# Kernel tuning notes

Measured on AMD Instinct MI355X. Metric: run time of the kernel, lower is better.

## Reference

```python
import jax, jax.numpy as jnp
import numpy as np

N_NODES = 100000
N_EDGES = 3200000
N_FEAT = 128
N_GRAPHS = 512
BN_EPS = 1e-5


def setup_inputs() -> dict:
    key = jax.random.key(0)
    ks = jax.random.split(key, 16)
    x = jax.random.normal(ks[0], (N_NODES, N_FEAT), dtype=jnp.float32)
    edge_index = jax.random.randint(ks[1], (2, N_EDGES), 0, N_NODES, dtype=jnp.int32)
    batch = jnp.sort(jax.random.randint(ks[2], (N_NODES,), 0, N_GRAPHS, dtype=jnp.int32))
    def lin(k, fi, fo):
        s = 1.0 / np.sqrt(fi)
        return jax.random.uniform(k, (fi, fo), jnp.float32, -s, s)
    return {
        "x": x,
        "edge_index": edge_index,
        "batch": batch,
        # conv1: GraphConv(128 -> 30): lin_rel (with bias) + lin_root (no bias)
        "W_rel1": lin(ks[3], N_FEAT, 30),
        "W_root1": lin(ks[4], N_FEAT, 30),
        "b1": jnp.zeros((30,), jnp.float32),
        "bn1_g": jnp.ones((30,), jnp.float32),
        "bn1_b": jnp.zeros((30,), jnp.float32),
        "bn1_m": jnp.zeros((30,), jnp.float32),
        "bn1_v": jnp.ones((30,), jnp.float32),
        # conv2: GraphConv(30 -> 20)
        "W_rel2": lin(ks[5], 30, 20),
        "W_root2": lin(ks[6], 30, 20),
        "b2": jnp.zeros((20,), jnp.float32),
        "bn2_g": jnp.ones((20,), jnp.float32),
        "bn2_b": jnp.zeros((20,), jnp.float32),
        "bn2_m": jnp.zeros((20,), jnp.float32),
        "bn2_v": jnp.ones((20,), jnp.float32),
        # head
        "W_lin1": lin(ks[7], 40, 10),
        "b_lin1": jnp.zeros((10,), jnp.float32),
        "W_lin2": lin(ks[8], 10, 1),
        "b_lin2": jnp.zeros((1,), jnp.float32),
    }


def _bn(h, g, b, m, v):
    return (h - m) * jax.lax.rsqrt(v + BN_EPS) * g + b


def reference(x, edge_index, batch,
              W_rel1, W_root1, b1, bn1_g, bn1_b, bn1_m, bn1_v,
              W_rel2, W_root2, b2, bn2_g, bn2_b, bn2_m, bn2_v,
              W_lin1, b_lin1, W_lin2, b_lin2):
    n = x.shape[0]
    src, dst = edge_index[0], edge_index[1]
    # ---- GraphConv 1: out = aggr_add(x_src -> dst) @ W_rel + x @ W_root + b
    agg = jax.ops.segment_sum(x[src], dst, num_segments=n)  # [N,128]
    h = jax.nn.relu(agg @ W_rel1 + x @ W_root1 + b1)        # [N,30]
    h = _bn(h, bn1_g, bn1_b, bn1_m, bn1_v)
    # ---- GraphConv 2
    agg2 = jax.ops.segment_sum(h[src], dst, num_segments=n)  # [N,30]
    h2 = jax.nn.relu(agg2 @ W_rel2 + h @ W_root2 + b2)       # [N,20]
    h2 = _bn(h2, bn2_g, bn2_b, bn2_m, bn2_v)
    # ---- global pools over graph ids
    gmax = jax.ops.segment_max(h2, batch, num_segments=N_GRAPHS)  # [G,20]
    gmax = jnp.where(jnp.isfinite(gmax), gmax, 0.0)
    gsum = jax.ops.segment_sum(h2, batch, num_segments=N_GRAPHS)
    cnt = jax.ops.segment_sum(jnp.ones((n,), h2.dtype), batch, num_segments=N_GRAPHS)
    gmean = gsum / jnp.maximum(cnt, 1.0)[:, None]
    z = jnp.concatenate([gmax, gmean], axis=1)               # [G,40]
    z = jax.nn.relu(z @ W_lin1 + b_lin1)
    return jax.nn.sigmoid(z @ W_lin2 + b_lin2)               # [G,1]
```

## Files before the change

kernel.cpp:

```cpp
#include <hip/hip_runtime.h>
#include <math.h>

#define NFEAT 128
#define F1    30
#define F1P   32
#define F2    20

#define EPB     8192
#define MAXBUCK 1024

__global__ __launch_bounds__(256) void k_prepw(
    const float* __restrict__ Wrel, const float* __restrict__ Wroot,
    float* __restrict__ Wp)
{
    int i = blockIdx.x * 256 + threadIdx.x;
    if (i >= 2 * 128 * 32) return;
    int table = i >> 12, rem = i & 4095, k = rem >> 5, j = rem & 31;
    const float* W = table ? Wroot : Wrel;
    Wp[i] = (j < F1) ? W[k * F1 + j] : 0.f;
}

__global__ __launch_bounds__(512) void k_proj1(
    const float* __restrict__ x, const float* __restrict__ Wp,
    float* __restrict__ y1, float* __restrict__ r1, int n)
{
    __shared__ float4 xs4[2048];
    int tid = threadIdx.x;
    int base = blockIdx.x * 64;

#pragma unroll
    for (int it = 0; it < 4; it++) {
        int idx = it * 512 + tid;
        int k4 = idx & 31, row = idx >> 5;
        int gnode = base + row;
        float4 v = make_float4(0.f, 0.f, 0.f, 0.f);
        if (gnode < n) v = ((const float4*)(x + (size_t)gnode * NFEAT))[k4];
        xs4[k4 * 64 + (row ^ k4)] = v;
    }
    __syncthreads();

    int lane = tid & 63;
    int combo = __builtin_amdgcn_readfirstlane(tid >> 6);
    int table = combo >> 2, q = combo & 3;
    int node = base + lane;
    if (node >= n) return;

    const float* Wt = Wp + table * 4096 + q * 8;
    float acc[8];
#pragma unroll
    for (int j = 0; j < 8; j++) acc[j] = 0.f;

    for (int k4 = 0; k4 < 32; k4++) {
        float4 xk = xs4[k4 * 64 + (lane ^ k4)];
#pragma unroll
        for (int kk = 0; kk < 4; kk++) {
            float xs = kk == 0 ? xk.x : kk == 1 ? xk.y : kk == 2 ? xk.z : xk.w;
            const float* w = Wt + (k4 * 4 + kk) * 32;
            acc[0] += xs * w[0]; acc[1] += xs * w[1];
            acc[2] += xs * w[2]; acc[3] += xs * w[3];
            acc[4] += xs * w[4]; acc[5] += xs * w[5];
            acc[6] += xs * w[6]; acc[7] += xs * w[7];
        }
    }
    float* outp = (table ? r1 : y1) + (size_t)node * F1P + q * 8;
    ((float4*)outp)[0] = make_float4(acc[0], acc[1], acc[2], acc[3]);
    ((float4*)outp)[1] = make_float4(acc[4], acc[5], acc[6], acc[7]);
}

__global__ __launch_bounds__(256) void k_p1(
    const int* __restrict__ ei, int* __restrict__ blockCnt,
    int E, int nbuck)
{
    __shared__ int lh[MAXBUCK];
    int t = threadIdx.x;
    for (int i = t; i < nbuck; i += 256) lh[i] = 0;
    __syncthreads();
    const int* dst = ei + E;
    int base = blockIdx.x * EPB;
#pragma unroll 4
    for (int k = 0; k < EPB / 256; k++) {
        int e = base + k * 256 + t;
        if (e < E) atomicAdd(&lh[dst[e] >> 7], 1);
    }
    __syncthreads();
    int* out = blockCnt + (size_t)blockIdx.x * nbuck;
    for (int i = t; i < nbuck; i += 256) out[i] = lh[i];
}

__global__ __launch_bounds__(256) void k_p2(
    const int* __restrict__ blockCnt, int* __restrict__ blockOff,
    int* __restrict__ bucketTot, int neb, int nbuck)
{
    __shared__ int sdata[256];
    __shared__ int carry_s;
    int b = blockIdx.x;
    int t = threadIdx.x;
    if (t == 0) carry_s = 0;
    __syncthreads();
    for (int base = 0; base < neb; base += 512) {
        int i0 = base + 2 * t, i1 = i0 + 1;
        int c0 = (i0 < neb) ? blockCnt[(size_t)i0 * nbuck + b] : 0;
        int c1 = (i1 < neb) ? blockCnt[(size_t)i1 * nbuck + b] : 0;
        int s = c0 + c1;
        sdata[t] = s;
        __syncthreads();
        for (int off = 1; off < 256; off <<= 1) {
            int tmp = (t >= off) ? sdata[t - off] : 0;
            __syncthreads();
            sdata[t] += tmp;
            __syncthreads();
        }
        int ex = carry_s + sdata[t] - s;
        if (i0 < neb) blockOff[(size_t)i0 * nbuck + b] = ex;
        if (i1 < neb) blockOff[(size_t)i1 * nbuck + b] = ex + c0;
        __syncthreads();
        if (t == 255) carry_s += sdata[255];
        __syncthreads();
    }
    if (t == 0) bucketTot[b] = carry_s;
}

__global__ __launch_bounds__(256) void k_p3(
    const int* __restrict__ bucketTot, int* __restrict__ bucketStart, int nbuck)
{
    __shared__ int sdata[256];
    __shared__ int carry_s;
    int t = threadIdx.x;
    if (t == 0) carry_s = 0;
    __syncthreads();
    for (int base = 0; base < nbuck; base += 1024) {
        int v[4]; int s = 0;
#pragma unroll
        for (int i = 0; i < 4; i++) {
            int idx = base + t * 4 + i;
            v[i] = (idx < nbuck) ? bucketTot[idx] : 0;
            s += v[i];
        }
        sdata[t] = s;
        __syncthreads();
        for (int off = 1; off < 256; off <<= 1) {
            int tmp = (t >= off) ? sdata[t - off] : 0;
            __syncthreads();
            sdata[t] += tmp;
            __syncthreads();
        }
        int ex = carry_s + sdata[t] - s;
#pragma unroll
        for (int i = 0; i < 4; i++) {
            int idx = base + t * 4 + i;
            if (idx < nbuck) bucketStart[idx] = ex;
            ex += v[i];
        }
        __syncthreads();
        if (t == 255) carry_s += sdata[255];
        __syncthreads();
    }
    if (t == 0) bucketStart[nbuck] = carry_s;
}

__global__ __launch_bounds__(256) void k_p4(
    const int* __restrict__ ei, const int* __restrict__ bucketStart,
    const int* __restrict__ blockOff, int* __restrict__ ebuf,
    int E, int nbuck)
{
    __shared__ int cur[MAXBUCK];
    int t = threadIdx.x;
    const int* boff = blockOff + (size_t)blockIdx.x * nbuck;
    for (int i = t; i < nbuck; i += 256) cur[i] = bucketStart[i] + boff[i];
    __syncthreads();
    const int* dst = ei + E;
    int base = blockIdx.x * EPB;
#pragma unroll 4
    for (int k = 0; k < EPB / 256; k++) {
        int e = base + k * 256 + t;
        if (e < E) {
            int s = ei[e], d = dst[e];
            int p = atomicAdd(&cur[d >> 7], 1);
            ebuf[p] = (s << 7) | (d & 127);
        }
    }
}

__global__ __launch_bounds__(256) void k_p5(
    const int* __restrict__ ebuf, const int* __restrict__ bucketStart,
    int* __restrict__ deg, int n)
{
    __shared__ int nh[128];
    int t = threadIdx.x;
    int b = blockIdx.x;
    if (t < 128) nh[t] = 0;
    __syncthreads();
    int lo = bucketStart[b], hi = bucketStart[b + 1];
    for (int p = lo + t; p < hi; p += 256)
        atomicAdd(&nh[ebuf[p] & 127], 1);
    __syncthreads();
    if (t < 128) {
        int node = b * 128 + t;
        if (node < n) deg[node] = nh[t];
    }
}

__global__ __launch_bounds__(256) void k_scan1(
    const int* __restrict__ deg, int* __restrict__ bsum, int n)
{
    __shared__ int sdata[256];
    int t = threadIdx.x;
    int base = blockIdx.x * 1024;
    int s = 0;
#pragma unroll
    for (int i = 0; i < 4; i++) {
        int idx = base + t * 4 + i;
        if (idx < n) s += deg[idx];
    }
    sdata[t] = s;
    __syncthreads();
    for (int off = 128; off > 0; off >>= 1) {
        if (t < off) sdata[t] += sdata[t + off];
        __syncthreads();
    }
    if (t == 0) bsum[blockIdx.x] = sdata[0];
}

__global__ void k_scan2(const int* __restrict__ bsum, int* __restrict__ boff, int nb)
{
    if (threadIdx.x == 0 && blockIdx.x == 0) {
        int acc = 0;
        for (int i = 0; i < nb; i++) { boff[i] = acc; acc += bsum[i]; }
    }
}

__global__ __launch_bounds__(256) void k_scan3(
    const int* __restrict__ deg, const int* __restrict__ boff,
    int* __restrict__ rowstart, int n)
{
    __shared__ int sdata[256];
    int t = threadIdx.x;
    int base = blockIdx.x * 1024;
    int v[4]; int s = 0;
#pragma unroll
    for (int i = 0; i < 4; i++) {
        int idx = base + t * 4 + i;
        v[i] = (idx < n) ? deg[idx] : 0;
        s += v[i];
    }
    sdata[t] = s;
    __syncthreads();
    for (int off = 1; off < 256; off <<= 1) {
        int tmp = (t >= off) ? sdata[t - off] : 0;
        __syncthreads();
        sdata[t] += tmp;
        __syncthreads();
    }
    int ex = boff[blockIdx.x] + sdata[t] - s;
#pragma unroll
    for (int i = 0; i < 4; i++) {
        int idx = base + t * 4 + i;
        if (idx < n) rowstart[idx] = ex;
        ex += v[i];
    }
}

__global__ __launch_bounds__(256) void k_p6(
    const int* __restrict__ ebuf, const int* __restrict__ bucketStart,
    const int* __restrict__ rowstart, int* __restrict__ perm, int n,
    int t1, int t2, int t3)
{
    __shared__ int cur[128];
    int t = threadIdx.x;
    int b = blockIdx.x;
    if (t < 128) {
        int node = b * 128 + t;
        cur[t] = (node < n) ? rowstart[node] : 0;
    }
    __syncthreads();
    int lo = bucketStart[b], hi = bucketStart[b + 1];
    for (int pass = 0; pass < 4; pass++) {
        for (int p = lo + t; p < hi; p += 256) {
            int e = ebuf[p];
            int src = e >> 7;
            int qq = (src >= t1) + (src >= t2) + (src >= t3);
            if (qq == pass) {
                int q = atomicAdd(&cur[e & 127], 1);
                perm[q] = src;
            }
        }
        __syncthreads();
    }
}

__global__ __launch_bounds__(256) void k_agg1(
    const int* __restrict__ rowstart, const int* __restrict__ deg,
    const int* __restrict__ perm, const float* __restrict__ y1,
    float* __restrict__ agg1, int n)
{
    int idx = blockIdx.x * 256 + threadIdx.x;
    int node = idx >> 3, q = idx & 7;
    if (node >= n) return;
    int s = rowstart[node], e = s + deg[node];
    float4 acc = {0.f, 0.f, 0.f, 0.f};
    int j = s;
    for (; j + 4 <= e; j += 4) {
        int s0 = perm[j], s1 = perm[j + 1], s2 = perm[j + 2], s3 = perm[j + 3];
        float4 v0 = *(const float4*)(y1 + (size_t)s0 * F1P + q * 4);
        float4 v1 = *(const float4*)(y1 + (size_t)s1 * F1P + q * 4);
        float4 v2 = *(const float4*)(y1 + (size_t)s2 * F1P + q * 4);
        float4 v3 = *(const float4*)(y1 + (size_t)s3 * F1P + q * 4);
        acc.x += v0.x; acc.y += v0.y; acc.z += v0.z; acc.w += v0.w;
        acc.x += v1.x; acc.y += v1.y; acc.z += v1.z; acc.w += v1.w;
        acc.x += v2.x; acc.y += v2.y; acc.z += v2.z; acc.w += v2.w;
        acc.x += v3.x; acc.y += v3.y; acc.z += v3.z; acc.w += v3.w;
    }
    for (; j < e; j++) {
        int sr = perm[j];
        float4 v = *(const float4*)(y1 + (size_t)sr * F1P + q * 4);
        acc.x += v.x; acc.y += v.y; acc.z += v.z; acc.w += v.w;
    }
    *(float4*)(agg1 + (size_t)node * F1P + q * 4) = acc;
}

__global__ __launch_bounds__(256) void k_agg2(
    const int* __restrict__ rowstart, const int* __restrict__ deg,
    const int* __restrict__ perm, const float* __restrict__ y2,
    float* __restrict__ agg2, int n)
{
    int idx = blockIdx.x * 256 + threadIdx.x;
    int node = idx / 5, q = idx - node * 5;
    if (node >= n) return;
    int s = rowstart[node], e = s + deg[node];
    float4 acc = {0.f, 0.f, 0.f, 0.f};
    int j = s;
    for (; j + 4 <= e; j += 4) {
        int s0 = perm[j], s1 = perm[j + 1], s2 = perm[j + 2], s3 = perm[j + 3];
        float4 v0 = *(const float4*)(y2 + (size_t)s0 * F2 + q * 4);
        float4 v1 = *(const float4*)(y2 + (size_t)s1 * F2 + q * 4);
        float4 v2 = *(const float4*)(y2 + (size_t)s2 * F2 + q * 4);
        float4 v3 = *(const float4*)(y2 + (size_t)s3 * F2 + q * 4);
        acc.x += v0.x; acc.y += v0.y; acc.z += v0.z; acc.w += v0.w;
        acc.x += v1.x; acc.y += v1.y; acc.z += v1.z; acc.w += v1.w;
        acc.x += v2.x; acc.y += v2.y; acc.z += v2.z; acc.w += v2.w;
        acc.x += v3.x; acc.y += v3.y; acc.z += v3.z; acc.w += v3.w;
    }
    for (; j < e; j++) {
        int sr = perm[j];
        float4 v = *(const float4*)(y2 + (size_t)sr * F2 + q * 4);
        acc.x += v.x; acc.y += v.y; acc.z += v.z; acc.w += v.w;
    }
    *(float4*)(agg2 + (size_t)node * F2 + q * 4) = acc;
}

__global__ __launch_bounds__(256) void k_mid(
    const float* __restrict__ agg1, const float* __restrict__ r1,
    const float* __restrict__ b1,
    const float* __restrict__ g1, const float* __restrict__ bb1,
    const float* __restrict__ m1, const float* __restrict__ v1,
    const float* __restrict__ Wrel2, const float* __restrict__ Wroot2,
    const float* __restrict__ b2,
    float* __restrict__ y2, float* __restrict__ r2, int n)
{
    int node = blockIdx.x * 256 + threadIdx.x;
    if (node >= n) return;
    float h[F1];
    const float4* av = (const float4*)(agg1 + (size_t)node * F1P);
    const float4* rv = (const float4*)(r1   + (size_t)node * F1P);
#pragma unroll
    for (int q = 0; q < 8; q++) {
        float4 a = av[q], r = rv[q];
        int j = q * 4;
        if (j + 0 < F1) h[j + 0] = a.x + r.x;
        if (j + 1 < F1) h[j + 1] = a.y + r.y;
        if (j + 2 < F1) h[j + 2] = a.z + r.z;
        if (j + 3 < F1) h[j + 3] = a.w + r.w;
    }
#pragma unroll
    for (int j = 0; j < F1; j++) {
        float t = fmaxf(h[j] + b1[j], 0.f);
        float sc = g1[j] / sqrtf(v1[j] + 1e-5f);
        h[j] = (t - m1[j]) * sc + bb1[j];
    }
    float ay[F2], ar[F2];
#pragma unroll
    for (int j = 0; j < F2; j++) { ay[j] = 0.f; ar[j] = b2[j]; }
    for (int k = 0; k < F1; k++) {
        float hk = h[k];
#pragma unroll
        for (int j = 0; j < F2; j++) {
            ay[j] += hk * Wrel2 [k * F2 + j];
            ar[j] += hk * Wroot2[k * F2 + j];
        }
    }
    float4* yo = (float4*)(y2 + (size_t)node * F2);
    float4* ro = (float4*)(r2 + (size_t)node * F2);
#pragma unroll
    for (int q = 0; q < 5; q++) {
        float4 vy, vr;
        vy.x = ay[q*4+0]; vy.y = ay[q*4+1]; vy.z = ay[q*4+2]; vy.w = ay[q*4+3];
        vr.x = ar[q*4+0]; vr.y = ar[q*4+1]; vr.z = ar[q*4+2]; vr.w = ar[q*4+3];
        yo[q] = vy;  ro[q] = vr;
    }
}

__global__ __launch_bounds__(256) void k_pool(
    const float* __restrict__ agg2, const float* __restrict__ r2,
    const int* __restrict__ batch,
    const float* __restrict__ g2, const float* __restrict__ bb2,
    const float* __restrict__ m2, const float* __restrict__ v2,
    unsigned* __restrict__ gmaxU, float* __restrict__ gsum,
    int* __restrict__ cnt, int n)
{
    int t = threadIdx.x;
    if (t >= 240) return;
    int i = t / 20, j = t - (t / 20) * 20;
    int base = blockIdx.x * 256;
    int nend = min(base + 256, n);
    float sc = g2[j] / sqrtf(v2[j] + 1e-5f);
    float mj = m2[j], bj = bb2[j];

    int curg = -1, c = 0;
    float mx = -3.4e38f, sm = 0.f;
    for (int node = base + i; node < nend; node += 12) {
        int g = batch[node];
        if (g != curg) {
            if (curg >= 0) {
                atomicAdd(&gsum[curg * F2 + j], sm);
                unsigned bits = __float_as_uint(mx);
                unsigned mapped = (bits & 0x80000000u) ? ~bits : (bits | 0x80000000u);
                atomicMax(&gmaxU[curg * F2 + j], mapped);
                if (j == 0) atomicAdd(&cnt[curg], c);
            }
            curg = g; c = 0; mx = -3.4e38f; sm = 0.f;
        }
        float a = agg2[(size_t)node * F2 + j] + r2[(size_t)node * F2 + j];
        a = fmaxf(a, 0.f);
        float h2 = (a - mj) * sc + bj;
        mx = fmaxf(mx, h2); sm += h2; c++;
    }
    if (curg >= 0) {
        atomicAdd(&gsum[curg * F2 + j], sm);
        unsigned bits = __float_as_uint(mx);
        unsigned mapped = (bits & 0x80000000u) ? ~bits : (bits | 0x80000000u);
        atomicMax(&gmaxU[curg * F2 + j], mapped);
        if (j == 0) atomicAdd(&cnt[curg], c);
    }
}

__global__ __launch_bounds__(256) void k_head(
    const unsigned* __restrict__ gmaxU, const float* __restrict__ gsum,
    const int* __restrict__ cnt,
    const float* __restrict__ W1, const float* __restrict__ b1h,
    const float* __restrict__ W2, const float* __restrict__ b2h,
    float* __restrict__ out, int G)
{
    int g = blockIdx.x * 256 + threadIdx.x;
    if (g >= G) return;
    int c = cnt[g];
    float cf = fmaxf((float)c, 1.f);
    float z[2 * F2];
#pragma unroll
    for (int j = 0; j < F2; j++) {
        unsigned u = gmaxU[g * F2 + j];
        float gm = 0.f;
        if (c != 0) {
            gm = (u & 0x80000000u) ? __uint_as_float(u & 0x7FFFFFFFu)
                                   : __uint_as_float(~u);
            if (!isfinite(gm)) gm = 0.f;
        }
        z[j]      = gm;
        z[F2 + j] = gsum[g * F2 + j] / cf;
    }
    float a[10];
#pragma unroll
    for (int i = 0; i < 10; i++) a[i] = b1h[i];
    for (int k = 0; k < 2 * F2; k++) {
        float zk = z[k];
#pragma unroll
        for (int i = 0; i < 10; i++) a[i] += zk * W1[k * 10 + i];
    }
    float o = b2h[0];
#pragma unroll
    for (int i = 0; i < 10; i++) o += fmaxf(a[i], 0.f) * W2[i];
    out[g] = 1.f / (1.f + expf(-o));
}

extern "C" void kernel_launch(void* const* d_in, const int* in_sizes, int n_in,
                              void* d_out, int out_size, void* d_ws, size_t ws_size,
                              hipStream_t stream)
{
    const float* x      = (const float*)d_in[0];
    const int*   ei     = (const int*)  d_in[1];
    const int*   batch  = (const int*)  d_in[2];
    const float* Wrel1  = (const float*)d_in[3];
    const float* Wroot1 = (const float*)d_in[4];
    const float* b1     = (const float*)d_in[5];
    const float* bn1_g  = (const float*)d_in[6];
    const float* bn1_b  = (const float*)d_in[7];
    const float* bn1_m  = (const float*)d_in[8];
    const float* bn1_v  = (const float*)d_in[9];
    const float* Wrel2  = (const float*)d_in[10];
    const float* Wroot2 = (const float*)d_in[11];
    const float* b2     = (const float*)d_in[12];
    const float* bn2_g  = (const float*)d_in[13];
    const float* bn2_b  = (const float*)d_in[14];
    const float* bn2_m  = (const float*)d_in[15];
    const float* bn2_v  = (const float*)d_in[16];
    const float* W_lin1 = (const float*)d_in[17];
    const float* b_lin1 = (const float*)d_in[18];
    const float* W_lin2 = (const float*)d_in[19];
    const float* b_lin2 = (const float*)d_in[20];
    float* out = (float*)d_out;

    int n = in_sizes[0] / NFEAT;
    int E = in_sizes[1] / 2;
    int G = out_size;
    int nb = (n + 1023) / 1024;
    int nbuck = (n + 127) >> 7;
    int neb = (E + EPB - 1) / EPB;
    int qs = (n + 3) >> 2;

    char* p = (char*)d_ws;
    float* y1   = (float*)p;  p += (size_t)n * F1P * 4;
    float* r1   = (float*)p;  p += (size_t)n * F1P * 4;
    char* alias0 = p;
    float* agg1 = (float*)p;  p += (size_t)n * F1P * 4;
    float* y2   = (float*)p;  p += (size_t)n * F2 * 4;
    float* r2   = (float*)p;  p += (size_t)n * F2 * 4;
    char* alias1 = p;
    float* agg2 = (float*)p;  p += (size_t)n * F2 * 4;
    unsigned* gmaxU = (unsigned*)p;  p += (size_t)G * F2 * 4;
    float*    gsum  = (float*)p;     p += (size_t)G * F2 * 4;
    int*      cnt   = (int*)p;       p += (size_t)G * 4;
    int* deg      = (int*)p;  p += (size_t)n * 4;
    int* rowstart = (int*)p;  p += (size_t)n * 4;
    int* bsum     = (int*)p;  p += (size_t)nb * 4;
    int* boff     = (int*)p;  p += (size_t)nb * 4;
    int* perm     = (int*)p;  p += (size_t)E * 4;
    float* Wp     = (float*)p; p += 2 * 128 * 32 * 4;

    int* ebuf = (int*)alias0;
    int* blockCnt    = (int*)alias1;
    int* blockOff    = blockCnt + (size_t)neb * nbuck;
    int* bucketTot   = blockOff + (size_t)neb * nbuck;
    int* bucketStart = bucketTot + nbuck;

    hipMemsetAsync(gmaxU, 0, (size_t)G * (F2 * 4 * 2 + 4), stream);

    k_p1<<<neb, 256, 0, stream>>>(ei, blockCnt, E, nbuck);
    k_p2<<<nbuck, 256, 0, stream>>>(blockCnt, blockOff, bucketTot, neb, nbuck);
    k_p3<<<1, 256, 0, stream>>>(bucketTot, bucketStart, nbuck);
    k_p4<<<neb, 256, 0, stream>>>(ei, bucketStart, blockOff, ebuf, E, nbuck);
    k_p5<<<nbuck, 256, 0, stream>>>(ebuf, bucketStart, deg, n);
    k_scan1<<<nb, 256, 0, stream>>>(deg, bsum, n);
    k_scan2<<<1, 64, 0, stream>>>(bsum, boff, nb);
    k_scan3<<<nb, 256, 0, stream>>>(deg, boff, rowstart, n);
    k_p6<<<nbuck, 256, 0, stream>>>(ebuf, bucketStart, rowstart, perm, n,
                                    qs, 2 * qs, 3 * qs);

    k_prepw<<<32, 256, 0, stream>>>(Wrel1, Wroot1, Wp);
    k_proj1<<<(n + 63) / 64, 512, 0, stream>>>(x, Wp, y1, r1, n);
    k_agg1<<<(n * 8 + 255) / 256, 256, 0, stream>>>(rowstart, deg, perm, y1, agg1, n);
    k_mid<<<(n + 255) / 256, 256, 0, stream>>>(agg1, r1, b1, bn1_g, bn1_b, bn1_m,
                                               bn1_v, Wrel2, Wroot2, b2, y2, r2, n);
    k_agg2<<<(n * 5 + 255) / 256, 256, 0, stream>>>(rowstart, deg, perm, y2, agg2, n);
    k_pool<<<(n + 255) / 256, 256, 0, stream>>>(agg2, r2, batch, bn2_g, bn2_b,
                                                bn2_m, bn2_v, gmaxU, gsum, cnt, n);
    k_head<<<(G + 255) / 256, 256, 0, stream>>>(gmaxU, gsum, cnt, W_lin1, b_lin1,
                                                W_lin2, b_lin2, out, G);
}
```

Measured before the change: 421.6 us.

## Replace global bucket sort with per-block local sort and transposed offsets

```diff
diff --git a/kernel.cpp b/kernel.cpp
--- a/kernel.cpp
+++ b/kernel.cpp
@@ -67,132 +67,87 @@
     ((float4*)outp)[1] = make_float4(acc[4], acc[5], acc[6], acc[7]);
 }
 
-__global__ __launch_bounds__(256) void k_p1(
-    const int* __restrict__ ei, int* __restrict__ blockCnt,
-    int E, int nbuck)
+__global__ __launch_bounds__(512) void k_sort(
+    const int* __restrict__ ei, int* __restrict__ ebuf,
+    int* __restrict__ rowScan, int E, int nbuck)
 {
     __shared__ int lh[MAXBUCK];
+    __shared__ int sdata[512];
     int t = threadIdx.x;
-    for (int i = t; i < nbuck; i += 256) lh[i] = 0;
-    __syncthreads();
+    int base = blockIdx.x * EPB;
+    const int* src = ei;
     const int* dst = ei + E;
-    int base = blockIdx.x * EPB;
+
+    for (int i = t; i < MAXBUCK; i += 512) lh[i] = 0;
+    __syncthreads();
 #pragma unroll 4
-    for (int k = 0; k < EPB / 256; k++) {
-        int e = base + k * 256 + t;
+    for (int k = 0; k < EPB / 512; k++) {
+        int e = base + k * 512 + t;
         if (e < E) atomicAdd(&lh[dst[e] >> 7], 1);
     }
     __syncthreads();
-    int* out = blockCnt + (size_t)blockIdx.x * nbuck;
-    for (int i = t; i < nbuck; i += 256) out[i] = lh[i];
-}
-
-__global__ __launch_bounds__(256) void k_p2(
-    const int* __restrict__ blockCnt, int* __restrict__ blockOff,
-    int* __restrict__ bucketTot, int neb, int nbuck)
-{
-    __shared__ int sdata[256];
-    __shared__ int carry_s;
-    int b = blockIdx.x;
-    int t = threadIdx.x;
-    if (t == 0) carry_s = 0;
-    __syncthreads();
-    for (int base = 0; base < neb; base += 512) {
-        int i0 = base + 2 * t, i1 = i0 + 1;
-        int c0 = (i0 < neb) ? blockCnt[(size_t)i0 * nbuck + b] : 0;
-        int c1 = (i1 < neb) ? blockCnt[(size_t)i1 * nbuck + b] : 0;
-        int s = c0 + c1;
-        sdata[t] = s;
+    int v0 = lh[2 * t], v1 = lh[2 * t + 1];
+    int pairSum = v0 + v1;
+    sdata[t] = pairSum;
+    __syncthreads();
+    for (int off = 1; off < 512; off <<= 1) {
+        int tmp = (t >= off) ? sdata[t - off] : 0;
         __syncthreads();
-        for (int off = 1; off < 256; off <<= 1) {
-            int tmp = (t >= off) ? sdata[t - off] : 0;
-            __syncthreads();
-            sdata[t] += tmp;
-            __syncthreads();
-        }
-        int ex = carry_s + sdata[t] - s;
-        if (i0 < neb) blockOff[(size_t)i0 * nbuck + b] = ex;
-        if (i1 < neb) blockOff[(size_t)i1 * nbuck + b] = ex + c0;
+        sdata[t] += tmp;
         __syncthreads();
-        if (t == 255) carry_s += sdata[255];
-        __syncthreads();
-    }
-    if (t == 0) bucketTot[b] = carry_s;
-}
-
-__global__ __launch_bounds__(256) void k_p3(
-    const int* __restrict__ bucketTot, int* __restrict__ bucketStart, int nbuck)
-{
-    __shared__ int sdata[256];
-    __shared__ int carry_s;
-    int t = threadIdx.x;
-    if (t == 0) carry_s = 0;
-    __syncthreads();
-    for (int base = 0; base < nbuck; base += 1024) {
-        int v[4]; int s = 0;
-#pragma unroll
-        for (int i = 0; i < 4; i++) {
-            int idx = base + t * 4 + i;
-            v[i] = (idx < nbuck) ? bucketTot[idx] : 0;
-            s += v[i];
-        }
-        sdata[t] = s;
-        __syncthreads();
-        for (int off = 1; off < 256; off <<= 1) {
-            int tmp = (t >= off) ? sdata[t - off] : 0;
-            __syncthreads();
-            sdata[t] += tmp;
-            __syncthreads();
-        }
-        int ex = carry_s + sdata[t] - s;
-#pragma unroll
-        for (int i = 0; i < 4; i++) {
-            int idx = base + t * 4 + i;
-            if (idx < nbuck) bucketStart[idx] = ex;
-            ex += v[i];
-        }
-        __syncthreads();
-        if (t == 255) carry_s += sdata[255];
-        __syncthreads();
-    }
-    if (t == 0) bucketStart[nbuck] = carry_s;
-}
-
-__global__ __launch_bounds__(256) void k_p4(
-    const int* __restrict__ ei, const int* __restrict__ bucketStart,
-    const int* __restrict__ blockOff, int* __restrict__ ebuf,
-    int E, int nbuck)
-{
-    __shared__ int cur[MAXBUCK];
-    int t = threadIdx.x;
-    const int* boff = blockOff + (size_t)blockIdx.x * nbuck;
-    for (int i = t; i < nbuck; i += 256) cur[i] = bucketStart[i] + boff[i];
-    __syncthreads();
-    const int* dst = ei + E;
-    int base = blockIdx.x * EPB;
+    }
+    int exPair = sdata[t] - pairSum;
+    lh[2 * t] = exPair;
+    lh[2 * t + 1] = exPair + v0;
+    __syncthreads();
+    int* rs = rowScan + (size_t)blockIdx.x * (nbuck + 1);
+    for (int i = t; i < nbuck + 1; i += 512) rs[i] = lh[i];
+    __syncthreads();
+    int* out = ebuf + (size_t)base;
 #pragma unroll 4
-    for (int k = 0; k < EPB / 256; k++) {
-        int e = base + k * 256 + t;
+    for (int k = 0; k < EPB / 512; k++) {
+        int e = base + k * 512 + t;
         if (e < E) {
-            int s = ei[e], d = dst[e];
-            int p = atomicAdd(&cur[d >> 7], 1);
-            ebuf[p] = (s << 7) | (d & 127);
-        }
+            int s = src[e], d = dst[e];
+            int p = atomicAdd(&lh[d >> 7], 1);
+            out[p] = (s << 7) | (d & 127);
+        }
+    }
+}
+
+__global__ __launch_bounds__(256) void k_t(
+    const int* __restrict__ in, int* __restrict__ out, int rows, int cols)
+{
+    __shared__ int tile[32][33];
+    int cb = blockIdx.x * 32, rb = blockIdx.y * 32;
+    for (int i = threadIdx.y; i < 32; i += 8) {
+        int r = rb + i, c = cb + threadIdx.x;
+        if (r < rows && c < cols) tile[i][threadIdx.x] = in[(size_t)r * cols + c];
+    }
+    __syncthreads();
+    for (int i = threadIdx.y; i < 32; i += 8) {
+        int c = cb + i, r = rb + threadIdx.x;
+        if (c < cols && r < rows) out[(size_t)c * rows + r] = tile[threadIdx.x][i];
     }
 }
 
 __global__ __launch_bounds__(256) void k_p5(
-    const int* __restrict__ ebuf, const int* __restrict__ bucketStart,
-    int* __restrict__ deg, int n)
+    const int* __restrict__ ebuf, const int* __restrict__ rsT,
+    int* __restrict__ deg, int n, int neb)
 {
     __shared__ int nh[128];
     int t = threadIdx.x;
     int b = blockIdx.x;
     if (t < 128) nh[t] = 0;
     __syncthreads();
-    int lo = bucketStart[b], hi = bucketStart[b + 1];
-    for (int p = lo + t; p < hi; p += 256)
-        atomicAdd(&nh[ebuf[p] & 127], 1);
+    const int* r0 = rsT + (size_t)b * neb;
+    const int* r1 = rsT + (size_t)(b + 1) * neb;
+    for (int blk = t; blk < neb; blk += 256) {
+        int lo = blk * EPB + r0[blk];
+        int hi = blk * EPB + r1[blk];
+        for (int p = lo; p < hi; p++)
+            atomicAdd(&nh[ebuf[p] & 127], 1);
+    }
     __syncthreads();
     if (t < 128) {
         int node = b * 128 + t;
@@ -261,9 +216,9 @@
 }
 
 __global__ __launch_bounds__(256) void k_p6(
-    const int* __restrict__ ebuf, const int* __restrict__ bucketStart,
-    const int* __restrict__ rowstart, int* __restrict__ perm, int n,
-    int t1, int t2, int t3)
+    const int* __restrict__ ebuf, const int* __restrict__ rsT,
+    const int* __restrict__ rowstart, int* __restrict__ perm,
+    int n, int neb, float inv8)
 {
     __shared__ int cur[128];
     int t = threadIdx.x;
@@ -272,14 +227,28 @@
         int node = b * 128 + t;
         cur[t] = (node < n) ? rowstart[node] : 0;
     }
-    __syncthreads();
-    int lo = bucketStart[b], hi = bucketStart[b + 1];
-    for (int pass = 0; pass < 4; pass++) {
-        for (int p = lo + t; p < hi; p += 256) {
+    const int* r0 = rsT + (size_t)b * neb;
+    const int* r1 = rsT + (size_t)(b + 1) * neb;
+    int blk0 = t, blk1 = t + 256;
+    int lo0 = 0, hi0 = 0, lo1 = 0, hi1 = 0;
+    if (blk0 < neb) { lo0 = blk0 * EPB + r0[blk0]; hi0 = blk0 * EPB + r1[blk0]; }
+    if (blk1 < neb) { lo1 = blk1 * EPB + r0[blk1]; hi1 = blk1 * EPB + r1[blk1]; }
+    __syncthreads();
+    for (int pass = 0; pass < 8; pass++) {
+        for (int p = lo0; p < hi0; p++) {
             int e = ebuf[p];
             int src = e >> 7;
-            int qq = (src >= t1) + (src >= t2) + (src >= t3);
-            if (qq == pass) {
+            int ph = min(7, (int)((float)src * inv8));
+            if (ph == pass) {
+                int q = atomicAdd(&cur[e & 127], 1);
+                perm[q] = src;
+            }
+        }
+        for (int p = lo1; p < hi1; p++) {
+            int e = ebuf[p];
+            int src = e >> 7;
+            int ph = min(7, (int)((float)src * inv8));
+            if (ph == pass) {
                 int q = atomicAdd(&cur[e & 127], 1);
                 perm[q] = src;
             }
@@ -514,7 +483,7 @@
     int nb = (n + 1023) / 1024;
     int nbuck = (n + 127) >> 7;
     int neb = (E + EPB - 1) / EPB;
-    int qs = (n + 3) >> 2;
+    float inv8 = 8.0f / (float)n;
 
     char* p = (char*)d_ws;
     float* y1   = (float*)p;  p += (size_t)n * F1P * 4;
@@ -535,24 +504,23 @@
     int* perm     = (int*)p;  p += (size_t)E * 4;
     float* Wp     = (float*)p; p += 2 * 128 * 32 * 4;
 
-    int* ebuf = (int*)alias0;
-    int* blockCnt    = (int*)alias1;
-    int* blockOff    = blockCnt + (size_t)neb * nbuck;
-    int* bucketTot   = blockOff + (size_t)neb * nbuck;
-    int* bucketStart = bucketTot + nbuck;
+    int* ebuf     = (int*)alias0;
+    int* rowScan  = (int*)alias1;
+    int* rowScanT = rowScan + (size_t)neb * (nbuck + 1);
 
     hipMemsetAsync(gmaxU, 0, (size_t)G * (F2 * 4 * 2 + 4), stream);
 
-    k_p1<<<neb, 256, 0, stream>>>(ei, blockCnt, E, nbuck);
-    k_p2<<<nbuck, 256, 0, stream>>>(blockCnt, blockOff, bucketTot, neb, nbuck);
-    k_p3<<<1, 256, 0, stream>>>(bucketTot, bucketStart, nbuck);
-    k_p4<<<neb, 256, 0, stream>>>(ei, bucketStart, blockOff, ebuf, E, nbuck);
-    k_p5<<<nbuck, 256, 0, stream>>>(ebuf, bucketStart, deg, n);
+    k_sort<<<neb, 512, 0, stream>>>(ei, ebuf, rowScan, E, nbuck);
+    {
+        dim3 tgrid((nbuck + 1 + 31) / 32, (neb + 31) / 32);
+        dim3 tblk(32, 8);
+        k_t<<<tgrid, tblk, 0, stream>>>(rowScan, rowScanT, neb, nbuck + 1);
+    }
+    k_p5<<<nbuck, 256, 0, stream>>>(ebuf, rowScanT, deg, n, neb);
     k_scan1<<<nb, 256, 0, stream>>>(deg, bsum, n);
     k_scan2<<<1, 64, 0, stream>>>(bsum, boff, nb);
     k_scan3<<<nb, 256, 0, stream>>>(deg, boff, rowstart, n);
-    k_p6<<<nbuck, 256, 0, stream>>>(ebuf, bucketStart, rowstart, perm, n,
-                                    qs, 2 * qs, 3 * qs);
+    k_p6<<<nbuck, 256, 0, stream>>>(ebuf, rowScanT, rowstart, perm, n, neb, inv8);
 
     k_prepw<<<32, 256, 0, stream>>>(Wrel1, Wroot1, Wp);
     k_proj1<<<(n + 63) / 64, 512, 0, stream>>>(x, Wp, y1, r1, n);
```

New measurement: 584.7 us. +38.7%, slower.

## Widen CSR buckets to 512 nodes, fuse degree scan, share neighbor indices via shuffles

Applied to the files above, without the earlier changes.

```diff
diff --git a/kernel.cpp b/kernel.cpp
--- a/kernel.cpp
+++ b/kernel.cpp
@@ -6,8 +6,8 @@
 #define F1P   32
 #define F2    20
 
-#define EPB     8192
-#define MAXBUCK 1024
+#define EPB   8192
+#define BW    512
 
 __global__ __launch_bounds__(256) void k_prepw(
     const float* __restrict__ Wrel, const float* __restrict__ Wroot,
@@ -67,24 +67,24 @@
     ((float4*)outp)[1] = make_float4(acc[4], acc[5], acc[6], acc[7]);
 }
 
-__global__ __launch_bounds__(256) void k_p1(
+__global__ __launch_bounds__(512) void k_p1(
     const int* __restrict__ ei, int* __restrict__ blockCnt,
     int E, int nbuck)
 {
-    __shared__ int lh[MAXBUCK];
-    int t = threadIdx.x;
-    for (int i = t; i < nbuck; i += 256) lh[i] = 0;
+    __shared__ int lh[256];
+    int t = threadIdx.x;
+    for (int i = t; i < 256; i += 512) lh[i] = 0;
     __syncthreads();
     const int* dst = ei + E;
     int base = blockIdx.x * EPB;
 #pragma unroll 4
-    for (int k = 0; k < EPB / 256; k++) {
-        int e = base + k * 256 + t;
-        if (e < E) atomicAdd(&lh[dst[e] >> 7], 1);
+    for (int k = 0; k < EPB / 512; k++) {
+        int e = base + k * 512 + t;
+        if (e < E) atomicAdd(&lh[dst[e] >> 9], 1);
     }
     __syncthreads();
     int* out = blockCnt + (size_t)blockIdx.x * nbuck;
-    for (int i = t; i < nbuck; i += 256) out[i] = lh[i];
+    for (int i = t; i < nbuck; i += 512) out[i] = lh[i];
 }
 
 __global__ __launch_bounds__(256) void k_p2(
@@ -124,126 +124,72 @@
     const int* __restrict__ bucketTot, int* __restrict__ bucketStart, int nbuck)
 {
     __shared__ int sdata[256];
-    __shared__ int carry_s;
-    int t = threadIdx.x;
-    if (t == 0) carry_s = 0;
-    __syncthreads();
-    for (int base = 0; base < nbuck; base += 1024) {
-        int v[4]; int s = 0;
-#pragma unroll
-        for (int i = 0; i < 4; i++) {
-            int idx = base + t * 4 + i;
-            v[i] = (idx < nbuck) ? bucketTot[idx] : 0;
-            s += v[i];
-        }
-        sdata[t] = s;
-        __syncthreads();
-        for (int off = 1; off < 256; off <<= 1) {
-            int tmp = (t >= off) ? sdata[t - off] : 0;
-            __syncthreads();
-            sdata[t] += tmp;
-            __syncthreads();
-        }
-        int ex = carry_s + sdata[t] - s;
-#pragma unroll
-        for (int i = 0; i < 4; i++) {
-            int idx = base + t * 4 + i;
-            if (idx < nbuck) bucketStart[idx] = ex;
-            ex += v[i];
-        }
-        __syncthreads();
-        if (t == 255) carry_s += sdata[255];
-        __syncthreads();
-    }
-    if (t == 0) bucketStart[nbuck] = carry_s;
-}
-
-__global__ __launch_bounds__(256) void k_p4(
+    int t = threadIdx.x;
+    int v[4]; int s = 0;
+#pragma unroll
+    for (int i = 0; i < 4; i++) {
+        int idx = t * 4 + i;
+        v[i] = (idx < nbuck) ? bucketTot[idx] : 0;
+        s += v[i];
+    }
+    sdata[t] = s;
+    __syncthreads();
+    for (int off = 1; off < 256; off <<= 1) {
+        int tmp = (t >= off) ? sdata[t - off] : 0;
+        __syncthreads();
+        sdata[t] += tmp;
+        __syncthreads();
+    }
+    int ex = sdata[t] - s;
+#pragma unroll
+    for (int i = 0; i < 4; i++) {
+        int idx = t * 4 + i;
+        if (idx < nbuck) bucketStart[idx] = ex;
+        ex += v[i];
+    }
+    if (t == 255) bucketStart[nbuck] = sdata[255];
+}
+
+__global__ __launch_bounds__(512) void k_p4(
     const int* __restrict__ ei, const int* __restrict__ bucketStart,
     const int* __restrict__ blockOff, int* __restrict__ ebuf,
     int E, int nbuck)
 {
-    __shared__ int cur[MAXBUCK];
+    __shared__ int cur[256];
     int t = threadIdx.x;
     const int* boff = blockOff + (size_t)blockIdx.x * nbuck;
-    for (int i = t; i < nbuck; i += 256) cur[i] = bucketStart[i] + boff[i];
+    for (int i = t; i < nbuck; i += 512) cur[i] = bucketStart[i] + boff[i];
     __syncthreads();
     const int* dst = ei + E;
     int base = blockIdx.x * EPB;
 #pragma unroll 4
-    for (int k = 0; k < EPB / 256; k++) {
-        int e = base + k * 256 + t;
+    for (int k = 0; k < EPB / 512; k++) {
+        int e = base + k * 512 + t;
         if (e < E) {
             int s = ei[e], d = dst[e];
-            int p = atomicAdd(&cur[d >> 7], 1);
-            ebuf[p] = (s << 7) | (d & 127);
+            int p = atomicAdd(&cur[d >> 9], 1);
+            ebuf[p] = (s << 9) | (d & 511);
         }
     }
 }
 
 __global__ __launch_bounds__(256) void k_p5(
     const int* __restrict__ ebuf, const int* __restrict__ bucketStart,
-    int* __restrict__ deg, int n)
-{
-    __shared__ int nh[128];
+    int* __restrict__ deg, int* __restrict__ rowstart, int n)
+{
+    __shared__ int nh[512];
+    __shared__ int sdata[256];
     int t = threadIdx.x;
     int b = blockIdx.x;
-    if (t < 128) nh[t] = 0;
+    nh[t] = 0; nh[t + 256] = 0;
     __syncthreads();
     int lo = bucketStart[b], hi = bucketStart[b + 1];
     for (int p = lo + t; p < hi; p += 256)
-        atomicAdd(&nh[ebuf[p] & 127], 1);
-    __syncthreads();
-    if (t < 128) {
-        int node = b * 128 + t;
-        if (node < n) deg[node] = nh[t];
-    }
-}
-
-__global__ __launch_bounds__(256) void k_scan1(
-    const int* __restrict__ deg, int* __restrict__ bsum, int n)
-{
-    __shared__ int sdata[256];
-    int t = threadIdx.x;
-    int base = blockIdx.x * 1024;
-    int s = 0;
-#pragma unroll
-    for (int i = 0; i < 4; i++) {
-        int idx = base + t * 4 + i;
-        if (idx < n) s += deg[idx];
-    }
-    sdata[t] = s;
-    __syncthreads();
-    for (int off = 128; off > 0; off >>= 1) {
-        if (t < off) sdata[t] += sdata[t + off];
-        __syncthreads();
-    }
-    if (t == 0) bsum[blockIdx.x] = sdata[0];
-}
-
-__global__ void k_scan2(const int* __restrict__ bsum, int* __restrict__ boff, int nb)
-{
-    if (threadIdx.x == 0 && blockIdx.x == 0) {
-        int acc = 0;
-        for (int i = 0; i < nb; i++) { boff[i] = acc; acc += bsum[i]; }
-    }
-}
-
-__global__ __launch_bounds__(256) void k_scan3(
-    const int* __restrict__ deg, const int* __restrict__ boff,
-    int* __restrict__ rowstart, int n)
-{
-    __shared__ int sdata[256];
-    int t = threadIdx.x;
-    int base = blockIdx.x * 1024;
-    int v[4]; int s = 0;
-#pragma unroll
-    for (int i = 0; i < 4; i++) {
-        int idx = base + t * 4 + i;
-        v[i] = (idx < n) ? deg[idx] : 0;
-        s += v[i];
-    }
-    sdata[t] = s;
+        atomicAdd(&nh[ebuf[p] & 511], 1);
+    __syncthreads();
+    int v0 = nh[2 * t], v1 = nh[2 * t + 1];
+    int ps = v0 + v1;
+    sdata[t] = ps;
     __syncthreads();
     for (int off = 1; off < 256; off <<= 1) {
         int tmp = (t >= off) ? sdata[t - off] : 0;
@@ -251,13 +197,10 @@
         sdata[t] += tmp;
         __syncthreads();
     }
-    int ex = boff[blockIdx.x] + sdata[t] - s;
-#pragma unroll
-    for (int i = 0; i < 4; i++) {
-        int idx = base + t * 4 + i;
-        if (idx < n) rowstart[idx] = ex;
-        ex += v[i];
-    }
+    int ex = sdata[t] - ps;
+    int n0 = b * BW + 2 * t, n1 = n0 + 1;
+    if (n0 < n) { rowstart[n0] = lo + ex;      deg[n0] = v0; }
+    if (n1 < n) { rowstart[n1] = lo + ex + v0; deg[n1] = v1; }
 }
 
 __global__ __launch_bounds__(256) void k_p6(
@@ -265,22 +208,21 @@
     const int* __restrict__ rowstart, int* __restrict__ perm, int n,
     int t1, int t2, int t3)
 {
-    __shared__ int cur[128];
+    __shared__ int cur[512];
     int t = threadIdx.x;
     int b = blockIdx.x;
-    if (t < 128) {
-        int node = b * 128 + t;
-        cur[t] = (node < n) ? rowstart[node] : 0;
-    }
+    int n0 = b * BW + t, n1 = n0 + 256;
+    cur[t]       = (n0 < n) ? rowstart[n0] : 0;
+    cur[t + 256] = (n1 < n) ? rowstart[n1] : 0;
     __syncthreads();
     int lo = bucketStart[b], hi = bucketStart[b + 1];
     for (int pass = 0; pass < 4; pass++) {
         for (int p = lo + t; p < hi; p += 256) {
             int e = ebuf[p];
-            int src = e >> 7;
+            int src = e >> 9;
             int qq = (src >= t1) + (src >= t2) + (src >= t3);
             if (qq == pass) {
-                int q = atomicAdd(&cur[e & 127], 1);
+                int q = atomicAdd(&cur[e & 511], 1);
                 perm[q] = src;
             }
         }
@@ -299,16 +241,14 @@
     int s = rowstart[node], e = s + deg[node];
     float4 acc = {0.f, 0.f, 0.f, 0.f};
     int j = s;
-    for (; j + 4 <= e; j += 4) {
-        int s0 = perm[j], s1 = perm[j + 1], s2 = perm[j + 2], s3 = perm[j + 3];
-        float4 v0 = *(const float4*)(y1 + (size_t)s0 * F1P + q * 4);
-        float4 v1 = *(const float4*)(y1 + (size_t)s1 * F1P + q * 4);
-        float4 v2 = *(const float4*)(y1 + (size_t)s2 * F1P + q * 4);
-        float4 v3 = *(const float4*)(y1 + (size_t)s3 * F1P + q * 4);
-        acc.x += v0.x; acc.y += v0.y; acc.z += v0.z; acc.w += v0.w;
-        acc.x += v1.x; acc.y += v1.y; acc.z += v1.z; acc.w += v1.w;
-        acc.x += v2.x; acc.y += v2.y; acc.z += v2.z; acc.w += v2.w;
-        acc.x += v3.x; acc.y += v3.y; acc.z += v3.z; acc.w += v3.w;
+    for (; j + 8 <= e; j += 8) {
+        int myp = perm[j + q];
+#pragma unroll
+        for (int k = 0; k < 8; k++) {
+            int sr = __shfl(myp, k, 8);
+            float4 v = *(const float4*)(y1 + (size_t)sr * F1P + q * 4);
+            acc.x += v.x; acc.y += v.y; acc.z += v.z; acc.w += v.w;
+        }
     }
     for (; j < e; j++) {
         int sr = perm[j];
@@ -324,28 +264,31 @@
     float* __restrict__ agg2, int n)
 {
     int idx = blockIdx.x * 256 + threadIdx.x;
-    int node = idx / 5, q = idx - node * 5;
+    int node = idx >> 3, q = idx & 7;
     if (node >= n) return;
+    bool valid = (q < 5);
     int s = rowstart[node], e = s + deg[node];
     float4 acc = {0.f, 0.f, 0.f, 0.f};
     int j = s;
-    for (; j + 4 <= e; j += 4) {
-        int s0 = perm[j], s1 = perm[j + 1], s2 = perm[j + 2], s3 = perm[j + 3];
-        float4 v0 = *(const float4*)(y2 + (size_t)s0 * F2 + q * 4);
-        float4 v1 = *(const float4*)(y2 + (size_t)s1 * F2 + q * 4);
-        float4 v2 = *(const float4*)(y2 + (size_t)s2 * F2 + q * 4);
-        float4 v3 = *(const float4*)(y2 + (size_t)s3 * F2 + q * 4);
-        acc.x += v0.x; acc.y += v0.y; acc.z += v0.z; acc.w += v0.w;
-        acc.x += v1.x; acc.y += v1.y; acc.z += v1.z; acc.w += v1.w;
-        acc.x += v2.x; acc.y += v2.y; acc.z += v2.z; acc.w += v2.w;
-        acc.x += v3.x; acc.y += v3.y; acc.z += v3.z; acc.w += v3.w;
-    }
-    for (; j < e; j++) {
-        int sr = perm[j];
-        float4 v = *(const float4*)(y2 + (size_t)sr * F2 + q * 4);
-        acc.x += v.x; acc.y += v.y; acc.z += v.z; acc.w += v.w;
-    }
-    *(float4*)(agg2 + (size_t)node * F2 + q * 4) = acc;
+    for (; j + 8 <= e; j += 8) {
+        int myp = perm[j + q];
+#pragma unroll
+        for (int k = 0; k < 8; k++) {
+            int sr = __shfl(myp, k, 8);
+            if (valid) {
+                float4 v = *(const float4*)(y2 + (size_t)sr * F2 + q * 4);
+                acc.x += v.x; acc.y += v.y; acc.z += v.z; acc.w += v.w;
+            }
+        }
+    }
+    if (valid) {
+        for (; j < e; j++) {
+            int sr = perm[j];
+            float4 v = *(const float4*)(y2 + (size_t)sr * F2 + q * 4);
+            acc.x += v.x; acc.y += v.y; acc.z += v.z; acc.w += v.w;
+        }
+        *(float4*)(agg2 + (size_t)node * F2 + q * 4) = acc;
+    }
 }
 
 __global__ __launch_bounds__(256) void k_mid(
@@ -511,8 +454,7 @@
     int n = in_sizes[0] / NFEAT;
     int E = in_sizes[1] / 2;
     int G = out_size;
-    int nb = (n + 1023) / 1024;
-    int nbuck = (n + 127) >> 7;
+    int nbuck = (n + BW - 1) / BW;
     int neb = (E + EPB - 1) / EPB;
     int qs = (n + 3) >> 2;
 
@@ -530,8 +472,6 @@
     int*      cnt   = (int*)p;       p += (size_t)G * 4;
     int* deg      = (int*)p;  p += (size_t)n * 4;
     int* rowstart = (int*)p;  p += (size_t)n * 4;
-    int* bsum     = (int*)p;  p += (size_t)nb * 4;
-    int* boff     = (int*)p;  p += (size_t)nb * 4;
     int* perm     = (int*)p;  p += (size_t)E * 4;
     float* Wp     = (float*)p; p += 2 * 128 * 32 * 4;
 
@@ -543,23 +483,20 @@
 
     hipMemsetAsync(gmaxU, 0, (size_t)G * (F2 * 4 * 2 + 4), stream);
 
-    k_p1<<<neb, 256, 0, stream>>>(ei, blockCnt, E, nbuck);
+    k_p1<<<neb, 512, 0, stream>>>(ei, blockCnt, E, nbuck);
     k_p2<<<nbuck, 256, 0, stream>>>(blockCnt, blockOff, bucketTot, neb, nbuck);
     k_p3<<<1, 256, 0, stream>>>(bucketTot, bucketStart, nbuck);
-    k_p4<<<neb, 256, 0, stream>>>(ei, bucketStart, blockOff, ebuf, E, nbuck);
-    k_p5<<<nbuck, 256, 0, stream>>>(ebuf, bucketStart, deg, n);
-    k_scan1<<<nb, 256, 0, stream>>>(deg, bsum, n);
-    k_scan2<<<1, 64, 0, stream>>>(bsum, boff, nb);
-    k_scan3<<<nb, 256, 0, stream>>>(deg, boff, rowstart, n);
+    k_p4<<<neb, 512, 0, stream>>>(ei, bucketStart, blockOff, ebuf, E, nbuck);
+    k_p5<<<nbuck, 256, 0, stream>>>(ebuf, bucketStart, deg, rowstart, n);
     k_p6<<<nbuck, 256, 0, stream>>>(ebuf, bucketStart, rowstart, perm, n,
                                     qs, 2 * qs, 3 * qs);
 
     k_prepw<<<32, 256, 0, stream>>>(Wrel1, Wroot1, Wp);
     k_proj1<<<(n + 63) / 64, 512, 0, stream>>>(x, Wp, y1, r1, n);
-    k_agg1<<<(n * 8 + 255) / 256, 256, 0, stream>>>(rowstart, deg, perm, y1, agg1, n);
+    k_agg1<<<((size_t)n * 8 + 255) / 256, 256, 0, stream>>>(rowstart, deg, perm, y1, agg1, n);
     k_mid<<<(n + 255) / 256, 256, 0, stream>>>(agg1, r1, b1, bn1_g, bn1_b, bn1_m,
                                                bn1_v, Wrel2, Wroot2, b2, y2, r2, n);
-    k_agg2<<<(n * 5 + 255) / 256, 256, 0, stream>>>(rowstart, deg, perm, y2, agg2, n);
+    k_agg2<<<((size_t)n * 8 + 255) / 256, 256, 0, stream>>>(rowstart, deg, perm, y2, agg2, n);
     k_pool<<<(n + 255) / 256, 256, 0, stream>>>(agg2, r2, batch, bn2_g, bn2_b,
                                                 bn2_m, bn2_v, gmaxU, gsum, cnt, n);
     k_head<<<(G + 255) / 256, 256, 0, stream>>>(gmaxU, gsum, cnt, W_lin1, b_lin1,
```

Result: slower. 465.3 us (+10.4%).
